# Optimization experiments

Measured on AMD Instinct MI355X. Metric: run time of the kernel, lower is better.

Reference implementation:

```python
import jax, jax.numpy as jnp
import numpy as np

LEAKY_SLOPE = 0.2


def _sample_ball(key, n, dim, radius):
    # uniform in unit ball: normalize gaussian, scale by U^(1/dim)
    k1, k2 = jax.random.split(key)
    g = jax.random.normal(k1, (n, dim), dtype=jnp.float32)
    g = g / jnp.linalg.norm(g, axis=-1, keepdims=True)
    r = jax.random.uniform(k2, (n, 1), dtype=jnp.float32) ** (1.0 / dim)
    return radius * g * r


def setup_inputs() -> dict:
    key = jax.random.key(0)
    ks = jax.random.split(key, 8)
    B, N, D, K = 16, 4096, 3, 4096
    IN, H1, H2, OUT = K + K * D, 1024, 512, 256
    point_cloud = jax.random.normal(ks[0], (B, N, D), dtype=jnp.float32) * 0.3
    basis = _sample_ball(ks[1], K, D, 1.0)
    s = 0.02
    W1 = jax.random.normal(ks[2], (IN, H1), dtype=jnp.float32) * s
    b1 = jnp.zeros((H1,), dtype=jnp.float32)
    W2 = jax.random.normal(ks[3], (H1, H2), dtype=jnp.float32) * s
    b2 = jnp.zeros((H2,), dtype=jnp.float32)
    W3 = jax.random.normal(ks[4], (H2, OUT), dtype=jnp.float32) * s
    b3 = jnp.zeros((OUT,), dtype=jnp.float32)
    return {"point_cloud": point_cloud, "basis": basis,
            "W1": W1, "b1": b1, "W2": W2, "b2": b2, "W3": W3, "b3": b3}


def _bps_encode(pc, basis):
    # pc: [B,N,3], basis: [K,3]
    # squared cdist via gemm expansion (avoids [B,K,N,3] broadcast)
    pn = jnp.sum(pc * pc, axis=-1)                     # [B,N]
    bn = jnp.sum(basis * basis, axis=-1)               # [K]
    cross = jnp.einsum('kd,bnd->bkn', basis, pc)       # [B,K,N]
    d2 = bn[None, :, None] + pn[:, None, :] - 2.0 * cross
    idx = jnp.argmin(d2, axis=-1)                      # [B,K]
    nearest = jnp.take_along_axis(pc, idx[..., None], axis=1)  # [B,K,3]
    deltas = nearest - basis[None, :, :]               # [B,K,3]
    dists = jnp.linalg.norm(deltas, axis=-1)           # [B,K]
    return dists, deltas


def reference(point_cloud, basis, W1, b1, W2, b2, W3, b3):
    B = point_cloud.shape[0]
    dists, deltas = _bps_encode(point_cloud, basis)
    bps_feature = jnp.concatenate([dists, deltas.reshape(B, -1)], axis=-1)  # [B, K+3K]
    h = bps_feature @ W1 + b1
    h = jnp.where(h >= 0, h, LEAKY_SLOPE * h)
    h = h @ W2 + b2
    h = jnp.where(h >= 0, h, LEAKY_SLOPE * h)
    global_feature = h @ W3 + b3
    return (global_feature, bps_feature[:, None, :])
```

## Files before the change

### kernel.cpp

```cpp
#include <hip/hip_runtime.h>

#define LEAKY_SLOPE 0.2f

constexpr int B_   = 16;
constexpr int N_   = 4096;
constexpr int K_   = 4096;
constexpr int IN_  = 16384;
constexpr int H1_  = 1024;
constexpr int H2_  = 512;
constexpr int OUT_ = 256;

constexpr int NCH = 64;
constexpr int NPC = N_ / NCH;
constexpr int KPT = 8;
constexpr int KTB = 256 * KPT;

__global__ __launch_bounds__(256) void enc_partial(
    const float* __restrict__ pc, const float* __restrict__ basis,
    float* __restrict__ chunkminf)
{
#pragma clang fp contract(off)
    __shared__ float4 pts[NPC + 1];
    const int kt = blockIdx.x;
    const int b  = blockIdx.y;
    const int c  = blockIdx.z;
    const int n0 = c * NPC;

    if (threadIdx.x < NPC) {
        const float* pp = pc + ((size_t)b * N_ + n0 + threadIdx.x) * 3;
        float x = pp[0], y = pp[1], z = pp[2];
        pts[threadIdx.x] = make_float4(x, y, z, (x * x + y * y) + z * z);
    }
    if (threadIdx.x == 0) pts[NPC] = make_float4(0.f, 0.f, 0.f, 0.f);
    __syncthreads();

    const int k0 = kt * KTB + (int)threadIdx.x;
    float nbx[KPT], nby[KPT], nbz[KPT], best[KPT];
#pragma unroll
    for (int q = 0; q < KPT; ++q) {
        int k = k0 + q * 256;
        nbx[q] = -2.0f * basis[k * 3 + 0];
        nby[q] = -2.0f * basis[k * 3 + 1];
        nbz[q] = -2.0f * basis[k * 3 + 2];
        best[q] = 3.4028235e38f;
    }

    float4 pcur = pts[0];
#pragma unroll 4
    for (int n = 0; n < NPC; ++n) {
        float4 pnext = pts[n + 1];
#pragma unroll
        for (int q = 0; q < KPT; ++q) {
            float e2 = __builtin_fmaf(nbx[q], pcur.x,
                        __builtin_fmaf(nby[q], pcur.y,
                         __builtin_fmaf(nbz[q], pcur.z, pcur.w)));
            best[q] = __builtin_fminf(best[q], e2);
        }
        pcur = pnext;
    }

    float* dst = chunkminf + ((size_t)(c * B_ + b)) * K_;
#pragma unroll
    for (int q = 0; q < KPT; ++q)
        dst[k0 + q * 256] = best[q];
}

__global__ __launch_bounds__(256) void enc_reduce_finish(
    const float* __restrict__ pc, const float* __restrict__ basis,
    const float* __restrict__ chunkminf,
    float* __restrict__ bps_out)
{
#pragma clang fp contract(off)
    const int t = blockIdx.x * 256 + (int)threadIdx.x;
    const int b = t >> 12;
    const int k = t & (K_ - 1);

    float m = 3.4028235e38f;
    int   cb = 0;
#pragma unroll 8
    for (int c = 0; c < NCH; ++c) {
        float v = chunkminf[((size_t)(c * B_ + b)) * K_ + k];
        if (v < m) { m = v; cb = c; }
    }

    const float bx0 = basis[k * 3 + 0];
    const float by0 = basis[k * 3 + 1];
    const float bz0 = basis[k * 3 + 2];
    const float nbx = -2.0f * bx0;
    const float nby = -2.0f * by0;
    const float nbz = -2.0f * bz0;

    const float4* pch = (const float4*)(pc + ((size_t)b * N_ + cb * NPC) * 3);
    float mm = 3.4028235e38f;
    float px = 0.f, py = 0.f, pz = 0.f;
#pragma unroll 4
    for (int g = 0; g < NPC / 4; ++g) {
        float4 q0 = pch[3 * g + 0];
        float4 q1 = pch[3 * g + 1];
        float4 q2 = pch[3 * g + 2];
        float xs[4] = { q0.x, q0.w, q1.z, q2.y };
        float ys[4] = { q0.y, q1.x, q1.w, q2.z };
        float zs[4] = { q0.z, q1.y, q2.x, q2.w };
#pragma unroll
        for (int j = 0; j < 4; ++j) {
            float x = xs[j], y = ys[j], z = zs[j];
            float pw = (x * x + y * y) + z * z;
            float e2 = __builtin_fmaf(nbx, x,
                        __builtin_fmaf(nby, y,
                         __builtin_fmaf(nbz, z, pw)));
            if (e2 < mm) { mm = e2; px = x; py = y; pz = z; }
        }
    }

    float dx = px - bx0;
    float dy = py - by0;
    float dz = pz - bz0;
    float dist = sqrtf((dx * dx + dy * dy) + dz * dz);

    float* row = bps_out + (size_t)b * IN_;
    row[k]              = dist;
    row[K_ + 3 * k + 0] = dx;
    row[K_ + 3 * k + 1] = dy;
    row[K_ + 3 * k + 2] = dz;
}

template<int ILEN, int NCOLS>
__global__ __launch_bounds__(256) void gemm1(
    const float* __restrict__ A, const float* __restrict__ W,
    float* __restrict__ part)
{
    __shared__ float red[4][64][33];
    const int lane = (int)threadIdx.x & 63;
    const int w    = __builtin_amdgcn_readfirstlane((int)threadIdx.x >> 6);
    const int j0   = blockIdx.x * 128 + lane * 2;
    const int i0   = blockIdx.y * ILEN + w * (ILEN / 4);

    float2 acc[16];
#pragma unroll
    for (int r = 0; r < 16; ++r) acc[r] = make_float2(0.f, 0.f);

#pragma unroll 4
    for (int i = i0; i < i0 + ILEN / 4; ++i) {
        float2 wv = *(const float2*)(W + (size_t)i * NCOLS + j0);
#pragma unroll
        for (int r = 0; r < 16; ++r) {
            float a = A[(size_t)r * IN_ + i];
            acc[r].x = __builtin_fmaf(a, wv.x, acc[r].x);
            acc[r].y = __builtin_fmaf(a, wv.y, acc[r].y);
        }
    }

#pragma unroll
    for (int r = 0; r < 16; ++r) {
        red[w][lane][2 * r]     = acc[r].x;
        red[w][lane][2 * r + 1] = acc[r].y;
    }
    __syncthreads();

    float* base = part + (size_t)blockIdx.y * 16 * NCOLS + blockIdx.x * 128 + lane * 2;
    const int b0 = w * 4;
#pragma unroll
    for (int b = b0; b < b0 + 4; ++b) {
        float sx = 0.f, sy = 0.f;
#pragma unroll
        for (int ww = 0; ww < 4; ++ww) {
            sx += red[ww][lane][2 * b];
            sy += red[ww][lane][2 * b + 1];
        }
        *(float2*)(base + (size_t)b * NCOLS) = make_float2(sx, sy);
    }
}

__global__ __launch_bounds__(256) void reduce_act1(
    const float* __restrict__ part, const float* __restrict__ bias,
    float* __restrict__ outT)
{
    const int p = blockIdx.x * 256 + (int)threadIdx.x;
    float s = 0.0f;
#pragma unroll 8
    for (int c = 0; c < 64; ++c) s += part[(size_t)c * (16 * H1_) + p];
    const int col = p & (H1_ - 1);
    const int b   = p >> 10;
    s += bias[col];
    s = fmaxf(s, LEAKY_SLOPE * s);
    outT[(size_t)col * 16 + b] = s;
}

template<int KDIM, int NCOLS>
__global__ __launch_bounds__(256) void gemm_mid(
    const float* __restrict__ AT, const float* __restrict__ W,
    float* __restrict__ part)
{
    __shared__ float red[4][64][17];
    const int lane = (int)threadIdx.x & 63;
    const int w    = __builtin_amdgcn_readfirstlane((int)threadIdx.x >> 6);
    const int cb   = blockIdx.x;
    const int s    = blockIdx.y;
    const int j    = cb * 64 + lane;
    constexpr int KS = KDIM / 8;
    constexpr int KW = KS / 4;
    const int i0 = s * KS + w * KW;

    float acc[16];
#pragma unroll
    for (int r = 0; r < 16; ++r) acc[r] = 0.0f;

#pragma unroll 4
    for (int i = i0; i < i0 + KW; ++i) {
        float wv = W[(size_t)i * NCOLS + j];
        const float4* Ar = (const float4*)(AT + (size_t)i * 16);
        float4 q0 = Ar[0], q1 = Ar[1], q2 = Ar[2], q3 = Ar[3];
        acc[0]  = __builtin_fmaf(q0.x, wv, acc[0]);
        acc[1]  = __builtin_fmaf(q0.y, wv, acc[1]);
        acc[2]  = __builtin_fmaf(q0.z, wv, acc[2]);
        acc[3]  = __builtin_fmaf(q0.w, wv, acc[3]);
        acc[4]  = __builtin_fmaf(q1.x, wv, acc[4]);
        acc[5]  = __builtin_fmaf(q1.y, wv, acc[5]);
        acc[6]  = __builtin_fmaf(q1.z, wv, acc[6]);
        acc[7]  = __builtin_fmaf(q1.w, wv, acc[7]);
        acc[8]  = __builtin_fmaf(q2.x, wv, acc[8]);
        acc[9]  = __builtin_fmaf(q2.y, wv, acc[9]);
        acc[10] = __builtin_fmaf(q2.z, wv, acc[10]);
        acc[11] = __builtin_fmaf(q2.w, wv, acc[11]);
        acc[12] = __builtin_fmaf(q3.x, wv, acc[12]);
        acc[13] = __builtin_fmaf(q3.y, wv, acc[13]);
        acc[14] = __builtin_fmaf(q3.z, wv, acc[14]);
        acc[15] = __builtin_fmaf(q3.w, wv, acc[15]);
    }

#pragma unroll
    for (int r = 0; r < 16; ++r) red[w][lane][r] = acc[r];
    __syncthreads();

#pragma unroll
    for (int q = 0; q < 4; ++q) {
        int p  = (int)threadIdx.x * 4 + q;
        int cl = p >> 4;
        int bt = p & 15;
        float ssum = 0.0f;
#pragma unroll
        for (int ww = 0; ww < 4; ++ww) ssum += red[ww][cl][bt];
        part[((size_t)s * NCOLS + cb * 64 + cl) * 16 + bt] = ssum;
    }
}

template<int KDIM, int NCOLS>
__global__ __launch_bounds__(256) void gemm_last(
    const float* __restrict__ h2part, const float* __restrict__ b2,
    const float* __restrict__ W, float* __restrict__ part)
{
    __shared__ float aT[64][20];
    __shared__ float red[4][64][17];
    const int lane = (int)threadIdx.x & 63;
    const int w    = __builtin_amdgcn_readfirstlane((int)threadIdx.x >> 6);
    const int cb   = blockIdx.x;
    const int s    = blockIdx.y;
    constexpr int KS = KDIM / 8;

    {
        const int il  = (int)threadIdx.x >> 2;
        const int btq = ((int)threadIdx.x & 3) * 4;
        const int i   = s * KS + il;
        float4 sum = make_float4(0.f, 0.f, 0.f, 0.f);
#pragma unroll
        for (int sl = 0; sl < 8; ++sl) {
            const float4 v = *(const float4*)(h2part +
                ((size_t)sl * H2_ + i) * 16 + btq);
            sum.x += v.x; sum.y += v.y; sum.z += v.z; sum.w += v.w;
        }
        const float bb = b2[i];
        sum.x += bb; sum.y += bb; sum.z += bb; sum.w += bb;
        sum.x = fmaxf(sum.x, LEAKY_SLOPE * sum.x);
        sum.y = fmaxf(sum.y, LEAKY_SLOPE * sum.y);
        sum.z = fmaxf(sum.z, LEAKY_SLOPE * sum.z);
        sum.w = fmaxf(sum.w, LEAKY_SLOPE * sum.w);
        *(float4*)&aT[il][btq] = sum;
    }
    __syncthreads();

    const int j  = cb * 64 + lane;
    const int i0 = w * 16;
    float acc[16];
#pragma unroll
    for (int r = 0; r < 16; ++r) acc[r] = 0.0f;

#pragma unroll 4
    for (int il = i0; il < i0 + 16; ++il) {
        float wv = W[((size_t)(s * KS + il)) * NCOLS + j];
        float4 q0 = *(const float4*)&aT[il][0];
        float4 q1 = *(const float4*)&aT[il][4];
        float4 q2 = *(const float4*)&aT[il][8];
        float4 q3 = *(const float4*)&aT[il][12];
        acc[0]  = __builtin_fmaf(q0.x, wv, acc[0]);
        acc[1]  = __builtin_fmaf(q0.y, wv, acc[1]);
        acc[2]  = __builtin_fmaf(q0.z, wv, acc[2]);
        acc[3]  = __builtin_fmaf(q0.w, wv, acc[3]);
        acc[4]  = __builtin_fmaf(q1.x, wv, acc[4]);
        acc[5]  = __builtin_fmaf(q1.y, wv, acc[5]);
        acc[6]  = __builtin_fmaf(q1.z, wv, acc[6]);
        acc[7]  = __builtin_fmaf(q1.w, wv, acc[7]);
        acc[8]  = __builtin_fmaf(q2.x, wv, acc[8]);
        acc[9]  = __builtin_fmaf(q2.y, wv, acc[9]);
        acc[10] = __builtin_fmaf(q2.z, wv, acc[10]);
        acc[11] = __builtin_fmaf(q2.w, wv, acc[11]);
        acc[12] = __builtin_fmaf(q3.x, wv, acc[12]);
        acc[13] = __builtin_fmaf(q3.y, wv, acc[13]);
        acc[14] = __builtin_fmaf(q3.z, wv, acc[14]);
        acc[15] = __builtin_fmaf(q3.w, wv, acc[15]);
    }

#pragma unroll
    for (int r = 0; r < 16; ++r) red[w][lane][r] = acc[r];
    __syncthreads();

#pragma unroll
    for (int q = 0; q < 4; ++q) {
        int p  = (int)threadIdx.x * 4 + q;
        int cl = p >> 4;
        int bt = p & 15;
        float ssum = 0.0f;
#pragma unroll
        for (int ww = 0; ww < 4; ++ww) ssum += red[ww][cl][bt];
        part[((size_t)s * NCOLS + cb * 64 + cl) * 16 + bt] = ssum;
    }
}

__global__ __launch_bounds__(256) void out_final(
    const float* __restrict__ h3part, const float* __restrict__ b3,
    float* __restrict__ out)
{
    const int t   = blockIdx.x * 256 + (int)threadIdx.x;
    const int col = t >> 4;
    const int bt  = t & 15;
    float s = b3[col];
#pragma unroll
    for (int sl = 0; sl < 8; ++sl)
        s += h3part[((size_t)sl * OUT_ + col) * 16 + bt];
    out[(size_t)bt * OUT_ + col] = s;
}

extern "C" void kernel_launch(void* const* d_in, const int* in_sizes, int n_in,
                              void* d_out, int out_size, void* d_ws, size_t ws_size,
                              hipStream_t stream)
{
    const float* pc    = (const float*)d_in[0];
    const float* basis = (const float*)d_in[1];
    const float* W1    = (const float*)d_in[2];
    const float* b1    = (const float*)d_in[3];
    const float* W2    = (const float*)d_in[4];
    const float* b2    = (const float*)d_in[5];
    const float* W3    = (const float*)d_in[6];
    const float* b3    = (const float*)d_in[7];

    float* out   = (float*)d_out;
    float* gfeat = out;
    float* bps   = out + B_ * OUT_;

    char* ws = (char*)d_ws;
    float* chunkminf = (float*)ws;
    float* partial = (float*)(ws + (size_t)16 * 1024 * 1024);
    float* h1T     = (float*)(ws + (size_t)20 * 1024 * 1024);
    float* h2part  = (float*)(ws + (size_t)20 * 1024 * 1024 + 64 * 1024);
    float* h3part  = (float*)(ws + (size_t)20 * 1024 * 1024 + 320 * 1024);

    enc_partial<<<dim3(K_ / KTB, B_, NCH), 256, 0, stream>>>(pc, basis, chunkminf);
    enc_reduce_finish<<<(B_ * K_) / 256, 256, 0, stream>>>(pc, basis, chunkminf, bps);
    gemm1<256, H1_><<<dim3(8, 64), 256, 0, stream>>>(bps, W1, partial);
    reduce_act1<<<(H1_ * 16) / 256, 256, 0, stream>>>(partial, b1, h1T);
    gemm_mid<1024, H2_><<<dim3(8, 8), 256, 0, stream>>>(h1T, W2, h2part);
    gemm_last<512, OUT_><<<dim3(4, 8), 256, 0, stream>>>(h2part, b2, W3, h3part);
    out_final<<<16, 256, 0, stream>>>(h3part, b3, gfeat);
}
```

Measured before the change: 170.9 us.

## Fuse MLP tail kernels into one cooperative kernel with grid syncs

```diff
diff --git a/kernel.cpp b/kernel.cpp
--- a/kernel.cpp
+++ b/kernel.cpp
@@ -1,4 +1,7 @@
 #include <hip/hip_runtime.h>
+#include <hip/hip_cooperative_groups.h>
+
+namespace cg = cooperative_groups;
 
 #define LEAKY_SLOPE 0.2f
 
@@ -171,172 +174,176 @@
     }
 }
 
-__global__ __launch_bounds__(256) void reduce_act1(
-    const float* __restrict__ part, const float* __restrict__ bias,
-    float* __restrict__ outT)
-{
-    const int p = blockIdx.x * 256 + (int)threadIdx.x;
-    float s = 0.0f;
+__global__ __launch_bounds__(256) void mlp_tail(
+    const float* __restrict__ part1, const float* __restrict__ b1,
+    const float* __restrict__ W2,    const float* __restrict__ b2,
+    const float* __restrict__ W3,    const float* __restrict__ b3,
+    float* __restrict__ h1T, float* __restrict__ h2part,
+    float* __restrict__ h3part, float* __restrict__ gfeat)
+{
+    __shared__ union {
+        float mid_red[4][64][17];
+        struct { float aT[64][20]; float red[4][64][17]; } last;
+    } sm;
+
+    cg::grid_group grid = cg::this_grid();
+    const int bid  = (int)blockIdx.x;
+    const int tid  = (int)threadIdx.x;
+    const int lane = tid & 63;
+    const int w    = __builtin_amdgcn_readfirstlane(tid >> 6);
+
+    {
+        const int p = bid * 256 + tid;
+        float s = 0.0f;
 #pragma unroll 8
-    for (int c = 0; c < 64; ++c) s += part[(size_t)c * (16 * H1_) + p];
-    const int col = p & (H1_ - 1);
-    const int b   = p >> 10;
-    s += bias[col];
-    s = fmaxf(s, LEAKY_SLOPE * s);
-    outT[(size_t)col * 16 + b] = s;
-}
-
-template<int KDIM, int NCOLS>
-__global__ __launch_bounds__(256) void gemm_mid(
-    const float* __restrict__ AT, const float* __restrict__ W,
-    float* __restrict__ part)
-{
-    __shared__ float red[4][64][17];
-    const int lane = (int)threadIdx.x & 63;
-    const int w    = __builtin_amdgcn_readfirstlane((int)threadIdx.x >> 6);
-    const int cb   = blockIdx.x;
-    const int s    = blockIdx.y;
-    const int j    = cb * 64 + lane;
-    constexpr int KS = KDIM / 8;
-    constexpr int KW = KS / 4;
-    const int i0 = s * KS + w * KW;
-
-    float acc[16];
-#pragma unroll
-    for (int r = 0; r < 16; ++r) acc[r] = 0.0f;
-
-#pragma unroll 4
-    for (int i = i0; i < i0 + KW; ++i) {
-        float wv = W[(size_t)i * NCOLS + j];
-        const float4* Ar = (const float4*)(AT + (size_t)i * 16);
-        float4 q0 = Ar[0], q1 = Ar[1], q2 = Ar[2], q3 = Ar[3];
-        acc[0]  = __builtin_fmaf(q0.x, wv, acc[0]);
-        acc[1]  = __builtin_fmaf(q0.y, wv, acc[1]);
-        acc[2]  = __builtin_fmaf(q0.z, wv, acc[2]);
-        acc[3]  = __builtin_fmaf(q0.w, wv, acc[3]);
-        acc[4]  = __builtin_fmaf(q1.x, wv, acc[4]);
-        acc[5]  = __builtin_fmaf(q1.y, wv, acc[5]);
-        acc[6]  = __builtin_fmaf(q1.z, wv, acc[6]);
-        acc[7]  = __builtin_fmaf(q1.w, wv, acc[7]);
-        acc[8]  = __builtin_fmaf(q2.x, wv, acc[8]);
-        acc[9]  = __builtin_fmaf(q2.y, wv, acc[9]);
-        acc[10] = __builtin_fmaf(q2.z, wv, acc[10]);
-        acc[11] = __builtin_fmaf(q2.w, wv, acc[11]);
-        acc[12] = __builtin_fmaf(q3.x, wv, acc[12]);
-        acc[13] = __builtin_fmaf(q3.y, wv, acc[13]);
-        acc[14] = __builtin_fmaf(q3.z, wv, acc[14]);
-        acc[15] = __builtin_fmaf(q3.w, wv, acc[15]);
-    }
-
-#pragma unroll
-    for (int r = 0; r < 16; ++r) red[w][lane][r] = acc[r];
-    __syncthreads();
-
-#pragma unroll
-    for (int q = 0; q < 4; ++q) {
-        int p  = (int)threadIdx.x * 4 + q;
-        int cl = p >> 4;
-        int bt = p & 15;
-        float ssum = 0.0f;
-#pragma unroll
-        for (int ww = 0; ww < 4; ++ww) ssum += red[ww][cl][bt];
-        part[((size_t)s * NCOLS + cb * 64 + cl) * 16 + bt] = ssum;
-    }
-}
-
-template<int KDIM, int NCOLS>
-__global__ __launch_bounds__(256) void gemm_last(
-    const float* __restrict__ h2part, const float* __restrict__ b2,
-    const float* __restrict__ W, float* __restrict__ part)
-{
-    __shared__ float aT[64][20];
-    __shared__ float red[4][64][17];
-    const int lane = (int)threadIdx.x & 63;
-    const int w    = __builtin_amdgcn_readfirstlane((int)threadIdx.x >> 6);
-    const int cb   = blockIdx.x;
-    const int s    = blockIdx.y;
-    constexpr int KS = KDIM / 8;
+        for (int c = 0; c < 64; ++c) s += part1[(size_t)c * (16 * H1_) + p];
+        const int col = p & (H1_ - 1);
+        const int b   = p >> 10;
+        s += b1[col];
+        s = fmaxf(s, LEAKY_SLOPE * s);
+        h1T[(size_t)col * 16 + b] = s;
+    }
+    __threadfence();
+    grid.sync();
 
     {
-        const int il  = (int)threadIdx.x >> 2;
-        const int btq = ((int)threadIdx.x & 3) * 4;
-        const int i   = s * KS + il;
-        float4 sum = make_float4(0.f, 0.f, 0.f, 0.f);
-#pragma unroll
-        for (int sl = 0; sl < 8; ++sl) {
-            const float4 v = *(const float4*)(h2part +
-                ((size_t)sl * H2_ + i) * 16 + btq);
-            sum.x += v.x; sum.y += v.y; sum.z += v.z; sum.w += v.w;
-        }
-        const float bb = b2[i];
-        sum.x += bb; sum.y += bb; sum.z += bb; sum.w += bb;
-        sum.x = fmaxf(sum.x, LEAKY_SLOPE * sum.x);
-        sum.y = fmaxf(sum.y, LEAKY_SLOPE * sum.y);
-        sum.z = fmaxf(sum.z, LEAKY_SLOPE * sum.z);
-        sum.w = fmaxf(sum.w, LEAKY_SLOPE * sum.w);
-        *(float4*)&aT[il][btq] = sum;
-    }
-    __syncthreads();
-
-    const int j  = cb * 64 + lane;
-    const int i0 = w * 16;
-    float acc[16];
-#pragma unroll
-    for (int r = 0; r < 16; ++r) acc[r] = 0.0f;
-
-#pragma unroll 4
-    for (int il = i0; il < i0 + 16; ++il) {
-        float wv = W[((size_t)(s * KS + il)) * NCOLS + j];
-        float4 q0 = *(const float4*)&aT[il][0];
-        float4 q1 = *(const float4*)&aT[il][4];
-        float4 q2 = *(const float4*)&aT[il][8];
-        float4 q3 = *(const float4*)&aT[il][12];
-        acc[0]  = __builtin_fmaf(q0.x, wv, acc[0]);
-        acc[1]  = __builtin_fmaf(q0.y, wv, acc[1]);
-        acc[2]  = __builtin_fmaf(q0.z, wv, acc[2]);
-        acc[3]  = __builtin_fmaf(q0.w, wv, acc[3]);
-        acc[4]  = __builtin_fmaf(q1.x, wv, acc[4]);
-        acc[5]  = __builtin_fmaf(q1.y, wv, acc[5]);
-        acc[6]  = __builtin_fmaf(q1.z, wv, acc[6]);
-        acc[7]  = __builtin_fmaf(q1.w, wv, acc[7]);
-        acc[8]  = __builtin_fmaf(q2.x, wv, acc[8]);
-        acc[9]  = __builtin_fmaf(q2.y, wv, acc[9]);
-        acc[10] = __builtin_fmaf(q2.z, wv, acc[10]);
-        acc[11] = __builtin_fmaf(q2.w, wv, acc[11]);
-        acc[12] = __builtin_fmaf(q3.x, wv, acc[12]);
-        acc[13] = __builtin_fmaf(q3.y, wv, acc[13]);
-        acc[14] = __builtin_fmaf(q3.z, wv, acc[14]);
-        acc[15] = __builtin_fmaf(q3.w, wv, acc[15]);
-    }
-
-#pragma unroll
-    for (int r = 0; r < 16; ++r) red[w][lane][r] = acc[r];
-    __syncthreads();
-
-#pragma unroll
-    for (int q = 0; q < 4; ++q) {
-        int p  = (int)threadIdx.x * 4 + q;
-        int cl = p >> 4;
-        int bt = p & 15;
-        float ssum = 0.0f;
-#pragma unroll
-        for (int ww = 0; ww < 4; ++ww) ssum += red[ww][cl][bt];
-        part[((size_t)s * NCOLS + cb * 64 + cl) * 16 + bt] = ssum;
-    }
-}
-
-__global__ __launch_bounds__(256) void out_final(
-    const float* __restrict__ h3part, const float* __restrict__ b3,
-    float* __restrict__ out)
-{
-    const int t   = blockIdx.x * 256 + (int)threadIdx.x;
-    const int col = t >> 4;
-    const int bt  = t & 15;
-    float s = b3[col];
-#pragma unroll
-    for (int sl = 0; sl < 8; ++sl)
-        s += h3part[((size_t)sl * OUT_ + col) * 16 + bt];
-    out[(size_t)bt * OUT_ + col] = s;
+        const int cb = bid & 7;
+        const int s  = bid >> 3;
+        const int j  = cb * 64 + lane;
+        constexpr int KS = H1_ / 8;
+        constexpr int KW = KS / 4;
+        const int i0 = s * KS + w * KW;
+
+        float acc[16];
+#pragma unroll
+        for (int r = 0; r < 16; ++r) acc[r] = 0.0f;
+
+#pragma unroll 4
+        for (int i = i0; i < i0 + KW; ++i) {
+            float wv = W2[(size_t)i * H2_ + j];
+            const float4* Ar = (const float4*)(h1T + (size_t)i * 16);
+            float4 q0 = Ar[0], q1 = Ar[1], q2 = Ar[2], q3 = Ar[3];
+            acc[0]  = __builtin_fmaf(q0.x, wv, acc[0]);
+            acc[1]  = __builtin_fmaf(q0.y, wv, acc[1]);
+            acc[2]  = __builtin_fmaf(q0.z, wv, acc[2]);
+            acc[3]  = __builtin_fmaf(q0.w, wv, acc[3]);
+            acc[4]  = __builtin_fmaf(q1.x, wv, acc[4]);
+            acc[5]  = __builtin_fmaf(q1.y, wv, acc[5]);
+            acc[6]  = __builtin_fmaf(q1.z, wv, acc[6]);
+            acc[7]  = __builtin_fmaf(q1.w, wv, acc[7]);
+            acc[8]  = __builtin_fmaf(q2.x, wv, acc[8]);
+            acc[9]  = __builtin_fmaf(q2.y, wv, acc[9]);
+            acc[10] = __builtin_fmaf(q2.z, wv, acc[10]);
+            acc[11] = __builtin_fmaf(q2.w, wv, acc[11]);
+            acc[12] = __builtin_fmaf(q3.x, wv, acc[12]);
+            acc[13] = __builtin_fmaf(q3.y, wv, acc[13]);
+            acc[14] = __builtin_fmaf(q3.z, wv, acc[14]);
+            acc[15] = __builtin_fmaf(q3.w, wv, acc[15]);
+        }
+
+#pragma unroll
+        for (int r = 0; r < 16; ++r) sm.mid_red[w][lane][r] = acc[r];
+        __syncthreads();
+
+#pragma unroll
+        for (int q = 0; q < 4; ++q) {
+            int p  = tid * 4 + q;
+            int cl = p >> 4;
+            int bt = p & 15;
+            float ssum = 0.0f;
+#pragma unroll
+            for (int ww = 0; ww < 4; ++ww) ssum += sm.mid_red[ww][cl][bt];
+            h2part[((size_t)s * H2_ + cb * 64 + cl) * 16 + bt] = ssum;
+        }
+    }
+    __threadfence();
+    grid.sync();
+
+    if (bid < 32) {
+        const int cb = bid & 3;
+        const int s  = bid >> 2;
+        constexpr int KS = H2_ / 8;
+
+        {
+            const int il  = tid >> 2;
+            const int btq = (tid & 3) * 4;
+            const int i   = s * KS + il;
+            float4 sum = make_float4(0.f, 0.f, 0.f, 0.f);
+#pragma unroll
+            for (int sl = 0; sl < 8; ++sl) {
+                const float4 v = *(const float4*)(h2part +
+                    ((size_t)sl * H2_ + i) * 16 + btq);
+                sum.x += v.x; sum.y += v.y; sum.z += v.z; sum.w += v.w;
+            }
+            const float bb = b2[i];
+            sum.x += bb; sum.y += bb; sum.z += bb; sum.w += bb;
+            sum.x = fmaxf(sum.x, LEAKY_SLOPE * sum.x);
+            sum.y = fmaxf(sum.y, LEAKY_SLOPE * sum.y);
+            sum.z = fmaxf(sum.z, LEAKY_SLOPE * sum.z);
+            sum.w = fmaxf(sum.w, LEAKY_SLOPE * sum.w);
+            *(float4*)&sm.last.aT[il][btq] = sum;
+        }
+        __syncthreads();
+
+        const int j  = cb * 64 + lane;
+        const int i0 = w * 16;
+        float acc[16];
+#pragma unroll
+        for (int r = 0; r < 16; ++r) acc[r] = 0.0f;
+
+#pragma unroll 4
+        for (int il = i0; il < i0 + 16; ++il) {
+            float wv = W3[((size_t)(s * KS + il)) * OUT_ + j];
+            float4 q0 = *(const float4*)&sm.last.aT[il][0];
+            float4 q1 = *(const float4*)&sm.last.aT[il][4];
+            float4 q2 = *(const float4*)&sm.last.aT[il][8];
+            float4 q3 = *(const float4*)&sm.last.aT[il][12];
+            acc[0]  = __builtin_fmaf(q0.x, wv, acc[0]);
+            acc[1]  = __builtin_fmaf(q0.y, wv, acc[1]);
+            acc[2]  = __builtin_fmaf(q0.z, wv, acc[2]);
+            acc[3]  = __builtin_fmaf(q0.w, wv, acc[3]);
+            acc[4]  = __builtin_fmaf(q1.x, wv, acc[4]);
+            acc[5]  = __builtin_fmaf(q1.y, wv, acc[5]);
+            acc[6]  = __builtin_fmaf(q1.z, wv, acc[6]);
+            acc[7]  = __builtin_fmaf(q1.w, wv, acc[7]);
+            acc[8]  = __builtin_fmaf(q2.x, wv, acc[8]);
+            acc[9]  = __builtin_fmaf(q2.y, wv, acc[9]);
+            acc[10] = __builtin_fmaf(q2.z, wv, acc[10]);
+            acc[11] = __builtin_fmaf(q2.w, wv, acc[11]);
+            acc[12] = __builtin_fmaf(q3.x, wv, acc[12]);
+            acc[13] = __builtin_fmaf(q3.y, wv, acc[13]);
+            acc[14] = __builtin_fmaf(q3.z, wv, acc[14]);
+            acc[15] = __builtin_fmaf(q3.w, wv, acc[15]);
+        }
+
+#pragma unroll
+        for (int r = 0; r < 16; ++r) sm.last.red[w][lane][r] = acc[r];
+        __syncthreads();
+
+#pragma unroll
+        for (int q = 0; q < 4; ++q) {
+            int p  = tid * 4 + q;
+            int cl = p >> 4;
+            int bt = p & 15;
+            float ssum = 0.0f;
+#pragma unroll
+            for (int ww = 0; ww < 4; ++ww) ssum += sm.last.red[ww][cl][bt];
+            h3part[((size_t)s * OUT_ + cb * 64 + cl) * 16 + bt] = ssum;
+        }
+    }
+    __threadfence();
+    grid.sync();
+
+    if (bid < 16) {
+        const int t   = bid * 256 + tid;
+        const int col = t >> 4;
+        const int bt  = t & 15;
+        float s = b3[col];
+#pragma unroll
+        for (int sl = 0; sl < 8; ++sl)
+            s += h3part[((size_t)sl * OUT_ + col) * 16 + bt];
+        gfeat[(size_t)bt * OUT_ + col] = s;
+    }
 }
 
 extern "C" void kernel_launch(void* const* d_in, const int* in_sizes, int n_in,
@@ -366,8 +373,13 @@
     enc_partial<<<dim3(K_ / KTB, B_, NCH), 256, 0, stream>>>(pc, basis, chunkminf);
     enc_reduce_finish<<<(B_ * K_) / 256, 256, 0, stream>>>(pc, basis, chunkminf, bps);
     gemm1<256, H1_><<<dim3(8, 64), 256, 0, stream>>>(bps, W1, partial);
-    reduce_act1<<<(H1_ * 16) / 256, 256, 0, stream>>>(partial, b1, h1T);
-    gemm_mid<1024, H2_><<<dim3(8, 8), 256, 0, stream>>>(h1T, W2, h2part);
-    gemm_last<512, OUT_><<<dim3(4, 8), 256, 0, stream>>>(h2part, b2, W3, h3part);
-    out_final<<<16, 256, 0, stream>>>(h3part, b3, gfeat);
-}
+    {
+        void* args[] = {
+            (void*)&partial, (void*)&b1, (void*)&W2, (void*)&b2,
+            (void*)&W3, (void*)&b3, (void*)&h1T, (void*)&h2part,
+            (void*)&h3part, (void*)&gfeat
+        };
+        hipLaunchCooperativeKernel((void*)mlp_tail, dim3(64), dim3(256),
+                                   args, 0, stream);
+    }
+}
```

Result: slower. 238.1 us (+39.3%).
